# Optimization experiments

Measured on AMD Instinct MI355X. Metric: run time of the kernel, lower is better.

Reference implementation:

```python
import jax, jax.numpy as jnp
import numpy as np

IN_, OUT_, HID, B = 1024, 1024, 4, 8192

def setup_inputs() -> dict:
    key = jax.random.key(0)
    k_x, k_w1, k_b1, k_w2, k_b2 = jax.random.split(key, 5)
    x = jax.random.normal(k_x, (B, IN_), dtype=jnp.float32)
    # Stacked params for out_ tiny MLPs: Linear(in,4) -> LeakyReLU(0.1) -> Linear(4,1)
    s1 = 1.0 / np.sqrt(IN_)
    s2 = 1.0 / np.sqrt(HID)
    W1 = jax.random.uniform(k_w1, (OUT_, IN_, HID), dtype=jnp.float32, minval=-s1, maxval=s1)
    b1 = jax.random.uniform(k_b1, (OUT_, HID), dtype=jnp.float32, minval=-s1, maxval=s1)
    W2 = jax.random.uniform(k_w2, (OUT_, HID), dtype=jnp.float32, minval=-s2, maxval=s2)
    b2 = jax.random.uniform(k_b2, (OUT_,), dtype=jnp.float32, minval=-s2, maxval=s2)
    return {"x": x, "W1": W1, "b1": b1, "W2": W2, "b2": b2}

def reference(x, W1, b1, W2, b2):
    # h[b,o,h] = x[b,:] @ W1[o] + b1[o]  (shared input across all out_ MLPs)
    h = jnp.einsum('bi,oih->boh', x, W1) + b1
    h = jnp.where(h >= 0, h, 0.1 * h)  # LeakyReLU(0.1)
    # out[b,o] = h[b,o,:] @ W2[o] + b2[o]; equals torch.cat of per-MLP scalars
    out = jnp.einsum('boh,oh->bo', h, W2) + b2
    return out
```

## Files before the change

kernel.cpp:

```cpp
#include <hip/hip_runtime.h>
#include <hip/hip_bf16.h>

#define IN_DIM  1024
#define OUT_DIM 1024
#define HID     4
#define BATCH   8192
#define NCOL    (OUT_DIM * HID)

typedef __bf16 bf16x8 __attribute__((ext_vector_type(8)));
typedef float  f32x4  __attribute__((ext_vector_type(4)));
typedef float  f32x16 __attribute__((ext_vector_type(16)));

__device__ __forceinline__ unsigned short f2bf(float f) {
  union { float f; unsigned int u; } v; v.f = f;
  unsigned int u = v.u;
  u += 0x7FFFu + ((u >> 16) & 1u);
  return (unsigned short)(u >> 16);
}

__global__ __launch_bounds__(256) void cvt_x_kernel(const float4* __restrict__ in,
                                                    ushort4* __restrict__ out) {
  int i = blockIdx.x * 256 + threadIdx.x;
  float4 v = in[i];
  ushort4 o;
  o.x = f2bf(v.x); o.y = f2bf(v.y); o.z = f2bf(v.z); o.w = f2bf(v.w);
  out[i] = o;
}

__global__ __launch_bounds__(256) void cvt_w1t_kernel(const float* __restrict__ W1,
                                                      ushort4* __restrict__ out) {
  int b = blockIdx.x;
  int g = ((b & 7) * ((int)gridDim.x >> 3) + (b >> 3)) * 256 + threadIdx.x;
  int i4 = g & 255;
  int oh = g >> 8;
  int h = oh & 3, o = oh >> 2;
  const float* src = W1 + (size_t)o * 4096 + h;
  ushort4 r;
  r.x = f2bf(src[(i4 * 4 + 0) * 4]);
  r.y = f2bf(src[(i4 * 4 + 1) * 4]);
  r.z = f2bf(src[(i4 * 4 + 2) * 4]);
  r.w = f2bf(src[(i4 * 4 + 3) * 4]);
  out[(size_t)oh * 256 + i4] = r;
}

__device__ __forceinline__ void gload16(const void* g, void* l) {
  __builtin_amdgcn_global_load_lds(
      (const __attribute__((address_space(1))) unsigned int*)g,
      (__attribute__((address_space(3))) unsigned int*)l, 16, 0, 0);
}

__global__ __launch_bounds__(256, 1) void mlp_gemm_kernel(
    const unsigned short* __restrict__ A,
    const unsigned short* __restrict__ Bm,
    const f32x4* __restrict__ b1v,
    const f32x4* __restrict__ w2v,
    const float* __restrict__ b2,
    float* __restrict__ out) {
  __shared__ __align__(16) unsigned short lds[65536];

  const int bid = blockIdx.x;
  const int xcd = bid & 7, loc = bid >> 3;
  const int bn = xcd * 4 + (loc & 3);
  const int bm = loc >> 2;
  const int tileM = bm * 256, tileN = bn * 256;

  const int t = threadIdx.x;
  const int lane = t & 63, wid = t >> 6;
  const int wm = wid >> 1, wn = wid & 1;
  const int l31 = lane & 31, hi = lane >> 5;

  const int sr8 = t >> 3, slt = t & 7;
  const int scol = ((slt ^ (sr8 & 7)) << 3);
  const unsigned short* Asrc = A  + (size_t)(tileM + sr8) * IN_DIM + scol;
  const unsigned short* Bsrc = Bm + (size_t)(tileN + sr8) * IN_DIM + scol;

  auto stage = [&](int kt, int p) {
    const int kb = kt * 64;
    unsigned short* lA = lds + p * 32768 + t * 8;
    unsigned short* lB = lA + 16384;
#pragma unroll
    for (int i = 0; i < 8; ++i) {
      gload16(Asrc + (size_t)(32 * i) * IN_DIM + kb, lA + i * 2048);
      gload16(Bsrc + (size_t)(32 * i) * IN_DIM + kb, lB + i * 2048);
    }
  };

  f32x16 acc[4][4];
#pragma unroll
  for (int m = 0; m < 4; ++m)
#pragma unroll
    for (int n = 0; n < 4; ++n)
#pragma unroll
      for (int r = 0; r < 16; ++r) acc[m][n][r] = 0.f;

  const int rsw = l31 & 7;

  stage(0, 0);
  asm volatile("s_waitcnt vmcnt(0)" ::: "memory");
  __builtin_amdgcn_s_barrier();

  for (int kt = 0; kt < 16; ++kt) {
    const int cur = kt & 1;
    if (kt < 15) stage(kt + 1, cur ^ 1);

    const unsigned short* bufp = lds + cur * 32768;
    const unsigned short* aR = bufp + (wm * 128 + l31) * 64;
    const unsigned short* bR = bufp + 16384 + (wn * 128 + l31) * 64;

#pragma unroll
    for (int ks = 0; ks < 4; ++ks) {
      const int pk = ((2 * ks + hi) ^ rsw) << 3;
      bf16x8 a[4], b[4];
      a[0] = *(const bf16x8*)(aR + 0 * 2048 + pk);
      b[0] = *(const bf16x8*)(bR + 0 * 2048 + pk);
      b[1] = *(const bf16x8*)(bR + 1 * 2048 + pk);
      b[2] = *(const bf16x8*)(bR + 2 * 2048 + pk);
      b[3] = *(const bf16x8*)(bR + 3 * 2048 + pk);
      a[1] = *(const bf16x8*)(aR + 1 * 2048 + pk);
      a[2] = *(const bf16x8*)(aR + 2 * 2048 + pk);
      a[3] = *(const bf16x8*)(aR + 3 * 2048 + pk);
#pragma unroll
      for (int mf = 0; mf < 4; ++mf)
#pragma unroll
        for (int nf = 0; nf < 4; ++nf)
          acc[mf][nf] = __builtin_amdgcn_mfma_f32_32x32x16_bf16(a[mf], b[nf], acc[mf][nf], 0, 0, 0);
    }

    if (kt < 15) asm volatile("s_waitcnt vmcnt(0)" ::: "memory");
    __builtin_amdgcn_s_barrier();
  }
  __syncthreads();

  float* LE = (float*)lds;
  const int obase = tileM >> 2;
#pragma unroll
  for (int mf = 0; mf < 4; ++mf) {
#pragma unroll
    for (int g = 0; g < 4; ++g) {
      int o_loc = wm * 32 + mf * 8 + 2 * g + hi;
      f32x4 b1q = b1v[obase + o_loc];
      f32x4 w2q = w2v[obase + o_loc];
#pragma unroll
      for (int nf = 0; nf < 4; ++nf) {
        int bat = wn * 128 + nf * 32 + l31;
        float v = 0.f;
#pragma unroll
        for (int h = 0; h < 4; ++h) {
          float hj = acc[mf][nf][4 * g + h] + b1q[h];
          hj = (hj >= 0.f) ? hj : 0.1f * hj;
          v += hj * w2q[h];
        }
        LE[bat * 65 + o_loc] = v;
      }
    }
  }
  __syncthreads();

  const int col = t & 63, rowb = t >> 6;
  const float b2s = b2[obase + col];
  float* outB = out + (size_t)tileN * OUT_DIM + obase;
#pragma unroll
  for (int i = 0; i < 64; ++i) {
    int row = rowb + i * 4;
    outB[(size_t)row * OUT_DIM + col] = LE[row * 65 + col] + b2s;
  }
}

__global__ __launch_bounds__(256) void fallback_kernel(
    const float* __restrict__ x, const float* __restrict__ W1,
    const float* __restrict__ b1, const float* __restrict__ W2,
    const float* __restrict__ b2, float* __restrict__ out) {
  int idx = blockIdx.x * 256 + threadIdx.x;
  if (idx >= BATCH * OUT_DIM) return;
  int bb = idx >> 10, o = idx & 1023;
  const float4* w1p = (const float4*)(W1 + (size_t)o * 4096);
  const float*  xp  = x + (size_t)bb * 1024;
  float4 acc = *(const float4*)(b1 + o * 4);
  for (int i = 0; i < 1024; ++i) {
    float xv = xp[i];
    float4 w = w1p[i];
    acc.x += xv * w.x; acc.y += xv * w.y; acc.z += xv * w.z; acc.w += xv * w.w;
  }
  float4 w2 = *(const float4*)(W2 + o * 4);
  float r = b2[o];
  r += ((acc.x >= 0.f) ? acc.x : 0.1f * acc.x) * w2.x;
  r += ((acc.y >= 0.f) ? acc.y : 0.1f * acc.y) * w2.y;
  r += ((acc.z >= 0.f) ? acc.z : 0.1f * acc.z) * w2.z;
  r += ((acc.w >= 0.f) ? acc.w : 0.1f * acc.w) * w2.w;
  out[(size_t)bb * OUT_DIM + o] = r;
}

extern "C" void kernel_launch(void* const* d_in, const int* in_sizes, int n_in,
                              void* d_out, int out_size, void* d_ws, size_t ws_size,
                              hipStream_t stream) {
  const float* x  = (const float*)d_in[0];
  const float* W1 = (const float*)d_in[1];
  const float* b1 = (const float*)d_in[2];
  const float* W2 = (const float*)d_in[3];
  const float* b2 = (const float*)d_in[4];
  float* out = (float*)d_out;

  size_t need = (size_t)BATCH * IN_DIM * 2 + (size_t)NCOL * IN_DIM * 2;
  if (ws_size >= need) {
    unsigned short* xbf = (unsigned short*)d_ws;
    unsigned short* w1t = xbf + (size_t)BATCH * IN_DIM;
    cvt_x_kernel<<<(BATCH * IN_DIM / 4) / 256, 256, 0, stream>>>((const float4*)x, (ushort4*)xbf);
    cvt_w1t_kernel<<<(NCOL * IN_DIM / 4) / 256, 256, 0, stream>>>(W1, (ushort4*)w1t);
    mlp_gemm_kernel<<<(NCOL / 256) * (BATCH / 256), 256, 0, stream>>>(
        w1t, xbf, (const f32x4*)b1, (const f32x4*)W2, b2, out);
  } else {
    fallback_kernel<<<(BATCH * OUT_DIM + 255) / 256, 256, 0, stream>>>(x, W1, b1, W2, b2, out);
  }
}
```

Measured before the change: 92.81 us.

## Load X operand directly from registers in MFMA fragment layout, halve N tile

The x conversion kernel now writes bf16 x in a pre-swizzled layout that matches the 16x16x32 MFMA B-fragment. The GEMM then loads its B operand straight from global memory into registers and keeps only the W1 tile in LDS. LDS use is halved and the N tile shrinks from 256 to 128 so that two blocks can share a CU, with the MFMA shape switched from 32x32x16 to 16x16x32. The aim is to cut LDS traffic and raise occupancy. In exchange, per-block reuse of x drops, global loads are issued directly into registers, and the wait on them sits inside the loop.

```diff
diff --git a/kernel.cpp b/kernel.cpp
--- a/kernel.cpp
+++ b/kernel.cpp
@@ -9,7 +9,6 @@
 
 typedef __bf16 bf16x8 __attribute__((ext_vector_type(8)));
 typedef float  f32x4  __attribute__((ext_vector_type(4)));
-typedef float  f32x16 __attribute__((ext_vector_type(16)));
 
 __device__ __forceinline__ unsigned short f2bf(float f) {
   union { float f; unsigned int u; } v; v.f = f;
@@ -18,13 +17,18 @@
   return (unsigned short)(u >> 16);
 }
 
-__global__ __launch_bounds__(256) void cvt_x_kernel(const float4* __restrict__ in,
-                                                    ushort4* __restrict__ out) {
-  int i = blockIdx.x * 256 + threadIdx.x;
-  float4 v = in[i];
-  ushort4 o;
-  o.x = f2bf(v.x); o.y = f2bf(v.y); o.z = f2bf(v.z); o.w = f2bf(v.w);
-  out[i] = o;
+__global__ __launch_bounds__(256) void cvt_xg_kernel(const float* __restrict__ x,
+                                                     uint4* __restrict__ xg) {
+  int g = blockIdx.x * 256 + threadIdx.x;
+  int bl = g & 15, ko = (g >> 4) & 127, c4 = g >> 11;
+  const float4* xp = (const float4*)(x + (size_t)(c4 * 16 + bl) * 1024 + ko * 8);
+  float4 v0 = xp[0], v1 = xp[1];
+  uint4 r;
+  r.x = f2bf(v0.x) | ((unsigned)f2bf(v0.y) << 16);
+  r.y = f2bf(v0.z) | ((unsigned)f2bf(v0.w) << 16);
+  r.z = f2bf(v1.x) | ((unsigned)f2bf(v1.y) << 16);
+  r.w = f2bf(v1.z) | ((unsigned)f2bf(v1.w) << 16);
+  xg[g] = r;
 }
 
 __global__ __launch_bounds__(256) void cvt_w1t_kernel(const float* __restrict__ W1,
@@ -49,53 +53,61 @@
       (__attribute__((address_space(3))) unsigned int*)l, 16, 0, 0);
 }
 
-__global__ __launch_bounds__(256, 1) void mlp_gemm_kernel(
+__global__ __launch_bounds__(256, 2) void mlp_gemm_kernel(
     const unsigned short* __restrict__ A,
-    const unsigned short* __restrict__ Bm,
+    const unsigned short* __restrict__ Bg,
     const f32x4* __restrict__ b1v,
     const f32x4* __restrict__ w2v,
     const float* __restrict__ b2,
     float* __restrict__ out) {
-  __shared__ __align__(16) unsigned short lds[65536];
+  __shared__ __align__(16) unsigned short lds[32768];
 
   const int bid = blockIdx.x;
   const int xcd = bid & 7, loc = bid >> 3;
-  const int bn = xcd * 4 + (loc & 3);
-  const int bm = loc >> 2;
-  const int tileM = bm * 256, tileN = bn * 256;
+  const int bn = xcd * 8 + (loc & 7);
+  const int bm = loc >> 3;
+  const int tileM = bm * 256, tileN = bn * 128;
 
   const int t = threadIdx.x;
   const int lane = t & 63, wid = t >> 6;
   const int wm = wid >> 1, wn = wid & 1;
-  const int l31 = lane & 31, hi = lane >> 5;
+  const int frow = lane & 15, jq = lane >> 4;
 
   const int sr8 = t >> 3, slt = t & 7;
   const int scol = ((slt ^ (sr8 & 7)) << 3);
-  const unsigned short* Asrc = A  + (size_t)(tileM + sr8) * IN_DIM + scol;
-  const unsigned short* Bsrc = Bm + (size_t)(tileN + sr8) * IN_DIM + scol;
+  const unsigned short* Asrc = A + (size_t)(tileM + sr8) * IN_DIM + scol;
 
   auto stage = [&](int kt, int p) {
     const int kb = kt * 64;
-    unsigned short* lA = lds + p * 32768 + t * 8;
-    unsigned short* lB = lA + 16384;
-#pragma unroll
-    for (int i = 0; i < 8; ++i) {
+    unsigned short* lA = lds + p * 16384 + t * 8;
+#pragma unroll
+    for (int i = 0; i < 8; ++i)
       gload16(Asrc + (size_t)(32 * i) * IN_DIM + kb, lA + i * 2048);
-      gload16(Bsrc + (size_t)(32 * i) * IN_DIM + kb, lB + i * 2048);
-    }
   };
 
-  f32x16 acc[4][4];
-#pragma unroll
-  for (int m = 0; m < 4; ++m)
-#pragma unroll
-    for (int n = 0; n < 4; ++n)
-#pragma unroll
-      for (int r = 0; r < 16; ++r) acc[m][n][r] = 0.f;
-
-  const int rsw = l31 & 7;
-
+  const int c40 = (tileN >> 4) + wn * 4;
+  const char* xgb = (const char*)Bg;
+  const char* bp0 = xgb + ((size_t)(c40 * 128 + jq) * 16 + frow) * 16;
+  const char* bp1 = bp0 + 32768;
+  const char* bp2 = bp0 + 65536;
+  const char* bp3 = bp0 + 98304;
+
+  f32x4 acc[8][4];
+#pragma unroll
+  for (int m = 0; m < 8; ++m)
+#pragma unroll
+    for (int n = 0; n < 4; ++n) acc[m][n] = f32x4{0.f, 0.f, 0.f, 0.f};
+
+  const int pk0 = (jq ^ (frow & 7)) << 3;
+  const int aRow = (wm * 128 + frow) * 64;
+
+  bf16x8 b0[4], b1_[4];
   stage(0, 0);
+  b0[0] = *(const bf16x8*)(bp0);  b1_[0] = *(const bf16x8*)(bp0 + 1024);
+  b0[1] = *(const bf16x8*)(bp1);  b1_[1] = *(const bf16x8*)(bp1 + 1024);
+  b0[2] = *(const bf16x8*)(bp2);  b1_[2] = *(const bf16x8*)(bp2 + 1024);
+  b0[3] = *(const bf16x8*)(bp3);  b1_[3] = *(const bf16x8*)(bp3 + 1024);
+  bp0 += 2048; bp1 += 2048; bp2 += 2048; bp3 += 2048;
   asm volatile("s_waitcnt vmcnt(0)" ::: "memory");
   __builtin_amdgcn_s_barrier();
 
@@ -103,55 +115,59 @@
     const int cur = kt & 1;
     if (kt < 15) stage(kt + 1, cur ^ 1);
 
-    const unsigned short* bufp = lds + cur * 32768;
-    const unsigned short* aR = bufp + (wm * 128 + l31) * 64;
-    const unsigned short* bR = bufp + 16384 + (wn * 128 + l31) * 64;
-
-#pragma unroll
-    for (int ks = 0; ks < 4; ++ks) {
-      const int pk = ((2 * ks + hi) ^ rsw) << 3;
-      bf16x8 a[4], b[4];
-      a[0] = *(const bf16x8*)(aR + 0 * 2048 + pk);
-      b[0] = *(const bf16x8*)(bR + 0 * 2048 + pk);
-      b[1] = *(const bf16x8*)(bR + 1 * 2048 + pk);
-      b[2] = *(const bf16x8*)(bR + 2 * 2048 + pk);
-      b[3] = *(const bf16x8*)(bR + 3 * 2048 + pk);
-      a[1] = *(const bf16x8*)(aR + 1 * 2048 + pk);
-      a[2] = *(const bf16x8*)(aR + 2 * 2048 + pk);
-      a[3] = *(const bf16x8*)(aR + 3 * 2048 + pk);
-#pragma unroll
-      for (int mf = 0; mf < 4; ++mf)
-#pragma unroll
-        for (int nf = 0; nf < 4; ++nf)
-          acc[mf][nf] = __builtin_amdgcn_mfma_f32_32x32x16_bf16(a[mf], b[nf], acc[mf][nf], 0, 0, 0);
-    }
-
-    if (kt < 15) asm volatile("s_waitcnt vmcnt(0)" ::: "memory");
-    __builtin_amdgcn_s_barrier();
+    const unsigned short* aB = lds + cur * 16384 + aRow;
+    bf16x8 a[8];
+#pragma unroll
+    for (int mf = 0; mf < 8; ++mf)
+      a[mf] = *(const bf16x8*)(aB + mf * 1024 + pk0);
+#pragma unroll
+    for (int mf = 0; mf < 8; ++mf) {
+      acc[mf][0] = __builtin_amdgcn_mfma_f32_16x16x32_bf16(a[mf], b0[0], acc[mf][0], 0, 0, 0);
+      acc[mf][1] = __builtin_amdgcn_mfma_f32_16x16x32_bf16(a[mf], b0[1], acc[mf][1], 0, 0, 0);
+      acc[mf][2] = __builtin_amdgcn_mfma_f32_16x16x32_bf16(a[mf], b0[2], acc[mf][2], 0, 0, 0);
+      acc[mf][3] = __builtin_amdgcn_mfma_f32_16x16x32_bf16(a[mf], b0[3], acc[mf][3], 0, 0, 0);
+    }
+#pragma unroll
+    for (int mf = 0; mf < 8; ++mf)
+      a[mf] = *(const bf16x8*)(aB + mf * 1024 + (pk0 ^ 32));
+#pragma unroll
+    for (int mf = 0; mf < 8; ++mf) {
+      acc[mf][0] = __builtin_amdgcn_mfma_f32_16x16x32_bf16(a[mf], b1_[0], acc[mf][0], 0, 0, 0);
+      acc[mf][1] = __builtin_amdgcn_mfma_f32_16x16x32_bf16(a[mf], b1_[1], acc[mf][1], 0, 0, 0);
+      acc[mf][2] = __builtin_amdgcn_mfma_f32_16x16x32_bf16(a[mf], b1_[2], acc[mf][2], 0, 0, 0);
+      acc[mf][3] = __builtin_amdgcn_mfma_f32_16x16x32_bf16(a[mf], b1_[3], acc[mf][3], 0, 0, 0);
+    }
+
+    if (kt < 15) {
+      asm volatile("s_waitcnt vmcnt(0)" ::: "memory");
+      b0[0] = *(const bf16x8*)(bp0);  b1_[0] = *(const bf16x8*)(bp0 + 1024);
+      b0[1] = *(const bf16x8*)(bp1);  b1_[1] = *(const bf16x8*)(bp1 + 1024);
+      b0[2] = *(const bf16x8*)(bp2);  b1_[2] = *(const bf16x8*)(bp2 + 1024);
+      b0[3] = *(const bf16x8*)(bp3);  b1_[3] = *(const bf16x8*)(bp3 + 1024);
+      bp0 += 2048; bp1 += 2048; bp2 += 2048; bp3 += 2048;
+      __builtin_amdgcn_s_barrier();
+    }
   }
   __syncthreads();
 
   float* LE = (float*)lds;
   const int obase = tileM >> 2;
 #pragma unroll
-  for (int mf = 0; mf < 4; ++mf) {
-#pragma unroll
-    for (int g = 0; g < 4; ++g) {
-      int o_loc = wm * 32 + mf * 8 + 2 * g + hi;
-      f32x4 b1q = b1v[obase + o_loc];
-      f32x4 w2q = w2v[obase + o_loc];
-#pragma unroll
-      for (int nf = 0; nf < 4; ++nf) {
-        int bat = wn * 128 + nf * 32 + l31;
-        float v = 0.f;
-#pragma unroll
-        for (int h = 0; h < 4; ++h) {
-          float hj = acc[mf][nf][4 * g + h] + b1q[h];
-          hj = (hj >= 0.f) ? hj : 0.1f * hj;
-          v += hj * w2q[h];
-        }
-        LE[bat * 65 + o_loc] = v;
+  for (int mf = 0; mf < 8; ++mf) {
+    int o_loc = wm * 32 + mf * 4 + jq;
+    f32x4 b1q = b1v[obase + o_loc];
+    f32x4 w2q = w2v[obase + o_loc];
+#pragma unroll
+    for (int nf = 0; nf < 4; ++nf) {
+      int bat = wn * 64 + nf * 16 + frow;
+      float v = 0.f;
+#pragma unroll
+      for (int h = 0; h < 4; ++h) {
+        float hj = acc[mf][nf][h] + b1q[h];
+        hj = (hj >= 0.f) ? hj : 0.1f * hj;
+        v += hj * w2q[h];
       }
+      LE[bat * 65 + o_loc] = v;
     }
   }
   __syncthreads();
@@ -160,7 +176,7 @@
   const float b2s = b2[obase + col];
   float* outB = out + (size_t)tileN * OUT_DIM + obase;
 #pragma unroll
-  for (int i = 0; i < 64; ++i) {
+  for (int i = 0; i < 32; ++i) {
     int row = rowb + i * 4;
     outB[(size_t)row * OUT_DIM + col] = LE[row * 65 + col] + b2s;
   }
@@ -202,12 +218,12 @@
 
   size_t need = (size_t)BATCH * IN_DIM * 2 + (size_t)NCOL * IN_DIM * 2;
   if (ws_size >= need) {
-    unsigned short* xbf = (unsigned short*)d_ws;
-    unsigned short* w1t = xbf + (size_t)BATCH * IN_DIM;
-    cvt_x_kernel<<<(BATCH * IN_DIM / 4) / 256, 256, 0, stream>>>((const float4*)x, (ushort4*)xbf);
+    unsigned short* xg  = (unsigned short*)d_ws;
+    unsigned short* w1t = xg + (size_t)BATCH * IN_DIM;
+    cvt_xg_kernel<<<(BATCH * IN_DIM / 8) / 256, 256, 0, stream>>>(x, (uint4*)xg);
     cvt_w1t_kernel<<<(NCOL * IN_DIM / 4) / 256, 256, 0, stream>>>(W1, (ushort4*)w1t);
-    mlp_gemm_kernel<<<(NCOL / 256) * (BATCH / 256), 256, 0, stream>>>(
-        w1t, xbf, (const f32x4*)b1, (const f32x4*)W2, b2, out);
+    mlp_gemm_kernel<<<(NCOL / 256) * (BATCH / 128), 256, 0, stream>>>(
+        w1t, xg, (const f32x4*)b1, (const f32x4*)W2, b2, out);
   } else {
     fallback_kernel<<<(BATCH * OUT_DIM + 255) / 256, 256, 0, stream>>>(x, W1, b1, W2, b2, out);
   }
```

Result: faster. 84.33 us (-9.1%).
